# Kernel tuning notes

Measured on AMD Instinct MI355X. Metric: run time of the kernel, lower is better.

Reference implementation:

```python
import jax, jax.numpy as jnp
import numpy as np

E = 512
H = 8
HD = E // H  # head dim = 64


def setup_inputs() -> dict:
    key = jax.random.key(0)
    ks = jax.random.split(key, 7)
    B, P, R = 32, 4096, 64
    visual_tokens = jax.random.normal(ks[0], (B, P, E), dtype=jnp.float32)
    region_tokens = jax.random.normal(ks[1], (B, R, E), dtype=jnp.float32)
    distance_mask = jax.random.uniform(ks[2], (B, P, R), dtype=jnp.float32)
    s = 1.0 / np.sqrt(E)
    in_proj_weight = jax.random.uniform(ks[3], (3 * E, E), jnp.float32, -s, s)
    in_proj_bias = jnp.zeros((3 * E,), jnp.float32)
    out_proj_weight = jax.random.uniform(ks[4], (E, E), jnp.float32, -s, s)
    out_proj_bias = jnp.zeros((E,), jnp.float32)
    return {
        "visual_tokens": visual_tokens,
        "region_tokens": region_tokens,
        "distance_mask": distance_mask,
        "in_proj_weight": in_proj_weight,
        "in_proj_bias": in_proj_bias,
        "out_proj_weight": out_proj_weight,
        "out_proj_bias": out_proj_bias,
    }


def reference(visual_tokens, region_tokens, distance_mask,
              in_proj_weight, in_proj_bias, out_proj_weight, out_proj_bias):
    B, P, _ = visual_tokens.shape
    R = region_tokens.shape[1]
    # additive logit bias derived from distance mask (broadcast over heads,
    # instead of repeating B*H copies like the torch code)
    bias = (1.0 - distance_mask.astype(jnp.float32)) * -1e9  # [B,P,R]
    Wq, Wk, Wv = in_proj_weight[:E], in_proj_weight[E:2 * E], in_proj_weight[2 * E:]
    bq, bk, bv = in_proj_bias[:E], in_proj_bias[E:2 * E], in_proj_bias[2 * E:]
    v32 = visual_tokens.astype(jnp.float32)
    r32 = region_tokens.astype(jnp.float32)
    q = (v32 @ Wq.T + bq).reshape(B, P, H, HD)
    k = (r32 @ Wk.T + bk).reshape(B, R, H, HD)
    v = (r32 @ Wv.T + bv).reshape(B, R, H, HD)
    scale = 1.0 / jnp.sqrt(jnp.float32(HD))
    scores = jnp.einsum('bphd,brhd->bhpr', q, k) * scale + bias[:, None]  # [B,H,P,R]
    attn = jax.nn.softmax(scores, axis=-1)
    ctx = jnp.einsum('bhpr,brhd->bphd', attn, v).reshape(B, P, E)
    attended = ctx @ out_proj_weight.T + out_proj_bias
    return attended.astype(visual_tokens.dtype) + visual_tokens
```

## Files before the change

### kernel.cpp

```cpp
#include <hip/hip_runtime.h>
#include <hip/hip_bf16.h>

typedef unsigned short u16;
typedef unsigned int u32;

using bf16x8 = __attribute__((ext_vector_type(8))) short;
using f32x4  = __attribute__((ext_vector_type(4))) float;

#define MFMA16(a, b, c) __builtin_amdgcn_mfma_f32_16x16x32_bf16((a), (b), (c), 0, 0, 0)

__device__ __forceinline__ u16 f2bf(float f) {
    u32 u = __builtin_bit_cast(u32, f);
    u = (u + 0x7fffu + ((u >> 16) & 1u)) >> 16;
    return (u16)u;
}

__global__ __launch_bounds__(256, 2) void frgca_prep(
    const float* __restrict__ region,
    const float* __restrict__ in_w,
    const float* __restrict__ in_b,
    const float* __restrict__ out_w,
    u16* __restrict__ wq, u16* __restrict__ wo,
    u16* __restrict__ kt, u16* __restrict__ vt)
{
    __shared__ u16 As2[64 * 520];
    const int tid = threadIdx.x;
    const int bid = blockIdx.x;

    if (bid < 32) {
        const float4* w4q = (const float4*)in_w;
        const float4* w4o = (const float4*)out_w;
        int t = bid * 256 + tid;
#pragma unroll
        for (int i = 0; i < 16; ++i) {
            int idx = t + i * 8192;
            float4 v;
            u16* dst;
            if (idx < 65536) { v = w4q[idx]; dst = wq + idx * 4; }
            else             { v = w4o[idx - 65536]; dst = wo + (idx - 65536) * 4; }
            ushort4 o;
            o.x = f2bf(v.x); o.y = f2bf(v.y); o.z = f2bf(v.z); o.w = f2bf(v.w);
            *(ushort4*)dst = o;
        }
        return;
    }

    const int t2 = bid - 32;
    const int b  = t2 >> 2;
    const int nc = t2 & 3;

    {
        const float4* r4 = (const float4*)(region + (size_t)b * 64 * 512);
#pragma unroll
        for (int i = 0; i < 32; ++i) {
            int f4  = tid + i * 256;
            int row = f4 >> 7;
            int c4  = f4 & 127;
            float4 v = r4[f4];
            ushort4 o;
            o.x = f2bf(v.x); o.y = f2bf(v.y); o.z = f2bf(v.z); o.w = f2bf(v.w);
            *(ushort4*)&As2[row * 520 + c4 * 4] = o;
        }
    }
    __syncthreads();

    const int lane = tid & 63, w = tid >> 6;
    const int lo16 = lane & 15, g = lane >> 4;
    const int e0 = nc * 256 + w * 64;

    f32x4 acc[4][4];
#pragma unroll
    for (int mt = 0; mt < 4; ++mt)
#pragma unroll
        for (int nt = 0; nt < 4; ++nt)
            acc[mt][nt] = f32x4{0.f, 0.f, 0.f, 0.f};

    const float* w2 = in_w + 512 * 512;

#pragma unroll 2
    for (int ks = 0; ks < 16; ++ks) {
        const int kc = ks * 32 + 8 * g;
        bf16x8 a[4], bb[4];
#pragma unroll
        for (int mt = 0; mt < 4; ++mt)
            a[mt] = *(const bf16x8*)&As2[(mt * 16 + lo16) * 520 + kc];
#pragma unroll
        for (int nt = 0; nt < 4; ++nt) {
            const int e = e0 + nt * 16 + lo16;
            const float* src = w2 + (size_t)e * 512 + kc;
            float4 v0 = *(const float4*)src;
            float4 v1 = *(const float4*)(src + 4);
            bf16x8 bv;
            bv[0] = (short)f2bf(v0.x); bv[1] = (short)f2bf(v0.y);
            bv[2] = (short)f2bf(v0.z); bv[3] = (short)f2bf(v0.w);
            bv[4] = (short)f2bf(v1.x); bv[5] = (short)f2bf(v1.y);
            bv[6] = (short)f2bf(v1.z); bv[7] = (short)f2bf(v1.w);
            bb[nt] = bv;
        }
#pragma unroll
        for (int mt = 0; mt < 4; ++mt)
#pragma unroll
            for (int nt = 0; nt < 4; ++nt)
                acc[mt][nt] = MFMA16(a[mt], bb[nt], acc[mt][nt]);
    }

#pragma unroll
    for (int nt = 0; nt < 4; ++nt) {
        const int e = e0 + nt * 16 + lo16;
        const float bias = in_b[512 + e];
#pragma unroll
        for (int mt = 0; mt < 4; ++mt)
#pragma unroll
            for (int i = 0; i < 4; ++i) {
                const int r = mt * 16 + 4 * g + i;
                const u16 o = f2bf(acc[mt][nt][i] + bias);
                if (e < 512) {
                    const int h = e >> 6, d = e & 63;
                    kt[(((size_t)(b * 8 + h)) * 64 + r) * 64 + d] = o;
                } else {
                    const int e2 = e - 512;
                    const int h = e2 >> 6, d = e2 & 63;
                    vt[(((size_t)(b * 8 + h)) * 64 + d) * 64 + r] = o;
                }
            }
    }
}

__global__ __launch_bounds__(512, 4) void frgca_main(
    const float* __restrict__ visual,
    const float* __restrict__ mask,
    const float* __restrict__ in_b,
    const float* __restrict__ out_b,
    const u16* __restrict__ wq, const u16* __restrict__ wo,
    const u16* __restrict__ kt, const u16* __restrict__ vt,
    float* __restrict__ out)
{
    __shared__ char regA[65536];
    __shared__ float Ms[4096];

    const int tid = threadIdx.x;
    const int w = tid >> 6, lane = tid & 63;
    const int lo16 = lane & 15, g = lane >> 4;
    const int xr = (lo16 & 7) << 4;
    const int pt = blockIdx.x, b = blockIdx.y;
    const int P0 = pt * 64;
    const size_t vbase = ((size_t)(b * 4096 + P0)) * 512;

    {
        const float4* v4 = (const float4*)(visual + vbase);
#pragma unroll
        for (int i = 0; i < 16; ++i) {
            int f4  = tid + i * 512;
            int row = f4 >> 7, c4 = f4 & 127;
            float4 v = v4[f4];
            ushort4 o;
            o.x = f2bf(v.x); o.y = f2bf(v.y); o.z = f2bf(v.z); o.w = f2bf(v.w);
            *(ushort4*)(regA + row * 1024 + ((c4 * 8) ^ ((row & 7) << 4))) = o;
        }
        const float4* m4 = (const float4*)(mask + ((size_t)(b * 4096 + P0)) * 64);
#pragma unroll
        for (int i = 0; i < 2; ++i) {
            int f4 = tid + i * 512;
            int p = f4 >> 4, r0 = (f4 & 15) * 4;
            float4 v = m4[f4];
            int pb = p * 64, px = p & 31;
            Ms[pb + ((r0 + 0) ^ px)] = (1.0f - v.x) * -1e9f;
            Ms[pb + ((r0 + 1) ^ px)] = (1.0f - v.y) * -1e9f;
            Ms[pb + ((r0 + 2) ^ px)] = (1.0f - v.z) * -1e9f;
            Ms[pb + ((r0 + 3) ^ px)] = (1.0f - v.w) * -1e9f;
        }
    }
    __syncthreads();

    const int e0 = w * 64;

    f32x4 acc[4][4];
#pragma unroll
    for (int mt = 0; mt < 4; ++mt)
#pragma unroll
        for (int nt = 0; nt < 4; ++nt)
            acc[mt][nt] = f32x4{0.f, 0.f, 0.f, 0.f};

    const u16* wqR0 = wq + ((size_t)(e0 + 0 * 16 + lo16)) * 512;
    const u16* wqR1 = wq + ((size_t)(e0 + 1 * 16 + lo16)) * 512;
    const u16* wqR2 = wq + ((size_t)(e0 + 2 * 16 + lo16)) * 512;
    const u16* wqR3 = wq + ((size_t)(e0 + 3 * 16 + lo16)) * 512;
    bf16x8 nb0 = *(const bf16x8*)&wqR0[8 * g];
    bf16x8 nb1 = *(const bf16x8*)&wqR1[8 * g];
    bf16x8 nb2 = *(const bf16x8*)&wqR2[8 * g];
    bf16x8 nb3 = *(const bf16x8*)&wqR3[8 * g];

#pragma unroll
    for (int ks = 0; ks < 16; ++ks) {
        const int kc = ks * 32 + 8 * g;
        bf16x8 cb0 = nb0, cb1 = nb1, cb2 = nb2, cb3 = nb3;
        if (ks < 15) {
            const int kn = kc + 32;
            nb0 = *(const bf16x8*)&wqR0[kn];
            nb1 = *(const bf16x8*)&wqR1[kn];
            nb2 = *(const bf16x8*)&wqR2[kn];
            nb3 = *(const bf16x8*)&wqR3[kn];
        }
        bf16x8 a[4];
#pragma unroll
        for (int mt = 0; mt < 4; ++mt)
            a[mt] = *(const bf16x8*)(regA + (mt * 16 + lo16) * 1024 + ((kc * 2) ^ xr));
        acc[0][0] = MFMA16(a[0], cb0, acc[0][0]);
        acc[1][0] = MFMA16(a[1], cb0, acc[1][0]);
        acc[2][0] = MFMA16(a[2], cb0, acc[2][0]);
        acc[3][0] = MFMA16(a[3], cb0, acc[3][0]);
        acc[0][1] = MFMA16(a[0], cb1, acc[0][1]);
        acc[1][1] = MFMA16(a[1], cb1, acc[1][1]);
        acc[2][1] = MFMA16(a[2], cb1, acc[2][1]);
        acc[3][1] = MFMA16(a[3], cb1, acc[3][1]);
        acc[0][2] = MFMA16(a[0], cb2, acc[0][2]);
        acc[1][2] = MFMA16(a[1], cb2, acc[1][2]);
        acc[2][2] = MFMA16(a[2], cb2, acc[2][2]);
        acc[3][2] = MFMA16(a[3], cb2, acc[3][2]);
        acc[0][3] = MFMA16(a[0], cb3, acc[0][3]);
        acc[1][3] = MFMA16(a[1], cb3, acc[1][3]);
        acc[2][3] = MFMA16(a[2], cb3, acc[2][3]);
        acc[3][3] = MFMA16(a[3], cb3, acc[3][3]);
    }

    const u16* KtH = kt + ((size_t)(b * 8 + w)) * 4096;
    bf16x8 ak[4][2];
#pragma unroll
    for (int ks2 = 0; ks2 < 2; ++ks2)
#pragma unroll
        for (int mt = 0; mt < 4; ++mt)
            ak[mt][ks2] = *(const bf16x8*)&KtH[(mt * 16 + lo16) * 64 + ks2 * 32 + 8 * g];

#pragma unroll
    for (int nt = 0; nt < 4; ++nt) {
        const float bq = in_b[e0 + nt * 16 + lo16];
#pragma unroll
        for (int mt = 0; mt < 4; ++mt)
#pragma unroll
            for (int i = 0; i < 4; ++i)
                acc[mt][nt][i] += bq;
    }
    __syncthreads();

    char* Qw = regA + w * 8192;
#pragma unroll
    for (int mt = 0; mt < 4; ++mt)
#pragma unroll
        for (int nt = 0; nt < 4; ++nt)
#pragma unroll
            for (int i = 0; i < 4; ++i) {
                const int p = mt * 16 + 4 * g + i;
                const int d = nt * 16 + lo16;
                *(u16*)(Qw + p * 128 + ((d * 2) ^ ((p & 7) << 4))) = f2bf(acc[mt][nt][i]);
            }

    f32x4 s[4][4];
#pragma unroll
    for (int mt = 0; mt < 4; ++mt)
#pragma unroll
        for (int nt = 0; nt < 4; ++nt)
            s[mt][nt] = f32x4{0.f, 0.f, 0.f, 0.f};

#pragma unroll
    for (int ks2 = 0; ks2 < 2; ++ks2) {
        const int kcb = (ks2 * 32 + 8 * g) * 2;
        bf16x8 bq_[4];
#pragma unroll
        for (int nt = 0; nt < 4; ++nt)
            bq_[nt] = *(const bf16x8*)(Qw + (nt * 16 + lo16) * 128 + (kcb ^ xr));
#pragma unroll
        for (int mt = 0; mt < 4; ++mt)
#pragma unroll
            for (int nt = 0; nt < 4; ++nt)
                s[mt][nt] = MFMA16(ak[mt][ks2], bq_[nt], s[mt][nt]);
    }

    const u16* VtH = vt + ((size_t)(b * 8 + w)) * 4096;
    bf16x8 av[4][2];
#pragma unroll
    for (int ks2 = 0; ks2 < 2; ++ks2)
#pragma unroll
        for (int mt = 0; mt < 4; ++mt)
            av[mt][ks2] = *(const bf16x8*)&VtH[(mt * 16 + lo16) * 64 + ks2 * 32 + 8 * g];

#pragma unroll
    for (int nt = 0; nt < 4; ++nt) {
        const int p = nt * 16 + lo16;
        const int pb = p * 64, px = p & 31;
        float mx = -3.4e38f;
#pragma unroll
        for (int mt = 0; mt < 4; ++mt)
#pragma unroll
            for (int i = 0; i < 4; ++i) {
                float v = s[mt][nt][i] * 0.125f + Ms[pb + ((mt * 16 + 4 * g + i) ^ px)];
                s[mt][nt][i] = v;
                mx = fmaxf(mx, v);
            }
        mx = fmaxf(mx, __shfl_xor(mx, 16));
        mx = fmaxf(mx, __shfl_xor(mx, 32));
        float sum = 0.f;
#pragma unroll
        for (int mt = 0; mt < 4; ++mt)
#pragma unroll
            for (int i = 0; i < 4; ++i) {
                float ev = __expf(s[mt][nt][i] - mx);
                s[mt][nt][i] = ev;
                sum += ev;
            }
        sum += __shfl_xor(sum, 16);
        sum += __shfl_xor(sum, 32);
        const float inv = 1.0f / sum;
#pragma unroll
        for (int mt = 0; mt < 4; ++mt)
#pragma unroll
            for (int i = 0; i < 4; ++i) {
                const int r = mt * 16 + 4 * g + i;
                *(u16*)(Qw + p * 128 + ((r * 2) ^ ((p & 7) << 4))) = f2bf(s[mt][nt][i] * inv);
            }
    }

    f32x4 c_[4][4];
#pragma unroll
    for (int mt = 0; mt < 4; ++mt)
#pragma unroll
        for (int nt = 0; nt < 4; ++nt)
            c_[mt][nt] = f32x4{0.f, 0.f, 0.f, 0.f};

#pragma unroll
    for (int ks2 = 0; ks2 < 2; ++ks2) {
        const int kcb = (ks2 * 32 + 8 * g) * 2;
        bf16x8 bs_[4];
#pragma unroll
        for (int nt = 0; nt < 4; ++nt)
            bs_[nt] = *(const bf16x8*)(Qw + (nt * 16 + lo16) * 128 + (kcb ^ xr));
#pragma unroll
        for (int mt = 0; mt < 4; ++mt)
#pragma unroll
            for (int nt = 0; nt < 4; ++nt)
                c_[mt][nt] = MFMA16(av[mt][ks2], bs_[nt], c_[mt][nt]);
    }
    __syncthreads();

#pragma unroll
    for (int mt = 0; mt < 4; ++mt)
#pragma unroll
        for (int nt = 0; nt < 4; ++nt)
#pragma unroll
            for (int i = 0; i < 4; ++i) {
                const int p = nt * 16 + lo16;
                const int c = e0 + mt * 16 + 4 * g + i;
                *(u16*)(regA + p * 1024 + ((c * 2) ^ ((p & 7) << 4))) = f2bf(c_[mt][nt][i]);
            }
    __syncthreads();

    f32x4 o_[4][4];
#pragma unroll
    for (int mt = 0; mt < 4; ++mt)
#pragma unroll
        for (int nt = 0; nt < 4; ++nt)
            o_[mt][nt] = f32x4{0.f, 0.f, 0.f, 0.f};

    const u16* woR0 = wo + ((size_t)(e0 + 0 * 16 + lo16)) * 512;
    const u16* woR1 = wo + ((size_t)(e0 + 1 * 16 + lo16)) * 512;
    const u16* woR2 = wo + ((size_t)(e0 + 2 * 16 + lo16)) * 512;
    const u16* woR3 = wo + ((size_t)(e0 + 3 * 16 + lo16)) * 512;
    bf16x8 ob0 = *(const bf16x8*)&woR0[8 * g];
    bf16x8 ob1 = *(const bf16x8*)&woR1[8 * g];
    bf16x8 ob2 = *(const bf16x8*)&woR2[8 * g];
    bf16x8 ob3 = *(const bf16x8*)&woR3[8 * g];

#pragma unroll
    for (int ks = 0; ks < 16; ++ks) {
        const int kc = ks * 32 + 8 * g;
        bf16x8 cb0 = ob0, cb1 = ob1, cb2 = ob2, cb3 = ob3;
        if (ks < 15) {
            const int kn = kc + 32;
            ob0 = *(const bf16x8*)&woR0[kn];
            ob1 = *(const bf16x8*)&woR1[kn];
            ob2 = *(const bf16x8*)&woR2[kn];
            ob3 = *(const bf16x8*)&woR3[kn];
        }
        bf16x8 a[4];
#pragma unroll
        for (int mt = 0; mt < 4; ++mt)
            a[mt] = *(const bf16x8*)(regA + (mt * 16 + lo16) * 1024 + ((kc * 2) ^ xr));
        o_[0][0] = MFMA16(a[0], cb0, o_[0][0]);
        o_[1][0] = MFMA16(a[1], cb0, o_[1][0]);
        o_[2][0] = MFMA16(a[2], cb0, o_[2][0]);
        o_[3][0] = MFMA16(a[3], cb0, o_[3][0]);
        o_[0][1] = MFMA16(a[0], cb1, o_[0][1]);
        o_[1][1] = MFMA16(a[1], cb1, o_[1][1]);
        o_[2][1] = MFMA16(a[2], cb1, o_[2][1]);
        o_[3][1] = MFMA16(a[3], cb1, o_[3][1]);
        o_[0][2] = MFMA16(a[0], cb2, o_[0][2]);
        o_[1][2] = MFMA16(a[1], cb2, o_[1][2]);
        o_[2][2] = MFMA16(a[2], cb2, o_[2][2]);
        o_[3][2] = MFMA16(a[3], cb2, o_[3][2]);
        o_[0][3] = MFMA16(a[0], cb3, o_[0][3]);
        o_[1][3] = MFMA16(a[1], cb3, o_[1][3]);
        o_[2][3] = MFMA16(a[2], cb3, o_[2][3]);
        o_[3][3] = MFMA16(a[3], cb3, o_[3][3]);
    }

#pragma unroll
    for (int nt = 0; nt < 4; ++nt) {
        const int e = e0 + nt * 16 + lo16;
        const float bo = out_b[e];
#pragma unroll
        for (int mt = 0; mt < 4; ++mt)
#pragma unroll
            for (int i = 0; i < 4; ++i) {
                const int p = mt * 16 + 4 * g + i;
                const size_t gid = vbase + (size_t)p * 512 + e;
                out[gid] = o_[mt][nt][i] + bo + visual[gid];
            }
    }
}

extern "C" void kernel_launch(void* const* d_in, const int* in_sizes, int n_in,
                              void* d_out, int out_size, void* d_ws, size_t ws_size,
                              hipStream_t stream) {
    const float* visual = (const float*)d_in[0];
    const float* region = (const float*)d_in[1];
    const float* mask   = (const float*)d_in[2];
    const float* in_w   = (const float*)d_in[3];
    const float* in_b   = (const float*)d_in[4];
    const float* out_w  = (const float*)d_in[5];
    const float* out_b  = (const float*)d_in[6];
    float* out = (float*)d_out;

    char* ws = (char*)d_ws;
    u16* wq = (u16*)(ws + 0);
    u16* wo = (u16*)(ws + 524288);
    u16* kt = (u16*)(ws + 1048576);
    u16* vt = (u16*)(ws + 3145728);

    frgca_prep<<<dim3(160), dim3(256), 0, stream>>>(region, in_w, in_b, out_w, wq, wo, kt, vt);
    frgca_main<<<dim3(64, 32), dim3(512), 0, stream>>>(visual, mask, in_b, out_b, wq, wo, kt, vt, out);
}
```

Before: 483.2 us.

## Split fused attention kernel into separate attention and output-projection kernels

Splits the monolithic main kernel into two launches. The first computes the Q projection, masked softmax attention and context, and writes the bf16 context per head to a workspace buffer. The second reloads that context and runs the output projection plus residual. The aim is probably to ease register or LDS pressure per kernel, at the cost of a 128MB round-trip through global memory and an extra launch. The old fused path remains as a fallback when the workspace is too small.

Result: slower. 632.2 us (+30.8%).

```diff
diff --git a/kernel.cpp b/kernel.cpp
--- a/kernel.cpp
+++ b/kernel.cpp
@@ -126,6 +126,308 @@
     }
 }
 
+__global__ __launch_bounds__(512, 4) void frgca_qattn(
+    const float* __restrict__ visual,
+    const float* __restrict__ mask,
+    const float* __restrict__ in_b,
+    const u16* __restrict__ wq,
+    const u16* __restrict__ kt, const u16* __restrict__ vt,
+    u16* __restrict__ cb)
+{
+    __shared__ char regA[65536];
+    __shared__ float Ms[4096];
+
+    const int tid = threadIdx.x;
+    const int w = tid >> 6, lane = tid & 63;
+    const int lo16 = lane & 15, g = lane >> 4;
+    const int xr = (lo16 & 7) << 4;
+    const int pt = blockIdx.x, b = blockIdx.y;
+    const int P0 = pt * 64;
+    const size_t vbase = ((size_t)(b * 4096 + P0)) * 512;
+
+    {
+        const float4* v4 = (const float4*)(visual + vbase);
+#pragma unroll
+        for (int i = 0; i < 16; ++i) {
+            int f4  = tid + i * 512;
+            int row = f4 >> 7, c4 = f4 & 127;
+            float4 v = v4[f4];
+            ushort4 o;
+            o.x = f2bf(v.x); o.y = f2bf(v.y); o.z = f2bf(v.z); o.w = f2bf(v.w);
+            *(ushort4*)(regA + row * 1024 + ((c4 * 8) ^ ((row & 7) << 4))) = o;
+        }
+        const float4* m4 = (const float4*)(mask + ((size_t)(b * 4096 + P0)) * 64);
+#pragma unroll
+        for (int i = 0; i < 2; ++i) {
+            int f4 = tid + i * 512;
+            int p = f4 >> 4, r0 = (f4 & 15) * 4;
+            float4 v = m4[f4];
+            int pb = p * 64, px = p & 31;
+            Ms[pb + ((r0 + 0) ^ px)] = (1.0f - v.x) * -1e9f;
+            Ms[pb + ((r0 + 1) ^ px)] = (1.0f - v.y) * -1e9f;
+            Ms[pb + ((r0 + 2) ^ px)] = (1.0f - v.z) * -1e9f;
+            Ms[pb + ((r0 + 3) ^ px)] = (1.0f - v.w) * -1e9f;
+        }
+    }
+    __syncthreads();
+
+    const int e0 = w * 64;
+
+    f32x4 acc[4][4];
+#pragma unroll
+    for (int mt = 0; mt < 4; ++mt)
+#pragma unroll
+        for (int nt = 0; nt < 4; ++nt)
+            acc[mt][nt] = f32x4{0.f, 0.f, 0.f, 0.f};
+
+    const u16* wqR0 = wq + ((size_t)(e0 + 0 * 16 + lo16)) * 512;
+    const u16* wqR1 = wq + ((size_t)(e0 + 1 * 16 + lo16)) * 512;
+    const u16* wqR2 = wq + ((size_t)(e0 + 2 * 16 + lo16)) * 512;
+    const u16* wqR3 = wq + ((size_t)(e0 + 3 * 16 + lo16)) * 512;
+    bf16x8 nb0 = *(const bf16x8*)&wqR0[8 * g];
+    bf16x8 nb1 = *(const bf16x8*)&wqR1[8 * g];
+    bf16x8 nb2 = *(const bf16x8*)&wqR2[8 * g];
+    bf16x8 nb3 = *(const bf16x8*)&wqR3[8 * g];
+
+#pragma unroll
+    for (int ks = 0; ks < 16; ++ks) {
+        const int kc = ks * 32 + 8 * g;
+        bf16x8 cb0 = nb0, cb1 = nb1, cb2 = nb2, cb3 = nb3;
+        if (ks < 15) {
+            const int kn = kc + 32;
+            nb0 = *(const bf16x8*)&wqR0[kn];
+            nb1 = *(const bf16x8*)&wqR1[kn];
+            nb2 = *(const bf16x8*)&wqR2[kn];
+            nb3 = *(const bf16x8*)&wqR3[kn];
+        }
+        bf16x8 a[4];
+#pragma unroll
+        for (int mt = 0; mt < 4; ++mt)
+            a[mt] = *(const bf16x8*)(regA + (mt * 16 + lo16) * 1024 + ((kc * 2) ^ xr));
+#pragma unroll
+        for (int mt = 0; mt < 4; ++mt) {
+            acc[mt][0] = MFMA16(a[mt], cb0, acc[mt][0]);
+            acc[mt][1] = MFMA16(a[mt], cb1, acc[mt][1]);
+            acc[mt][2] = MFMA16(a[mt], cb2, acc[mt][2]);
+            acc[mt][3] = MFMA16(a[mt], cb3, acc[mt][3]);
+        }
+    }
+
+    const u16* KtH = kt + ((size_t)(b * 8 + w)) * 4096;
+    bf16x8 ak[4][2];
+#pragma unroll
+    for (int ks2 = 0; ks2 < 2; ++ks2)
+#pragma unroll
+        for (int mt = 0; mt < 4; ++mt)
+            ak[mt][ks2] = *(const bf16x8*)&KtH[(mt * 16 + lo16) * 64 + ks2 * 32 + 8 * g];
+
+#pragma unroll
+    for (int nt = 0; nt < 4; ++nt) {
+        const float bq = in_b[e0 + nt * 16 + lo16];
+#pragma unroll
+        for (int mt = 0; mt < 4; ++mt)
+#pragma unroll
+            for (int i = 0; i < 4; ++i)
+                acc[mt][nt][i] += bq;
+    }
+    __syncthreads();
+
+    char* Qw = regA + w * 8192;
+#pragma unroll
+    for (int mt = 0; mt < 4; ++mt)
+#pragma unroll
+        for (int nt = 0; nt < 4; ++nt)
+#pragma unroll
+            for (int i = 0; i < 4; ++i) {
+                const int p = mt * 16 + 4 * g + i;
+                const int d = nt * 16 + lo16;
+                *(u16*)(Qw + p * 128 + ((d * 2) ^ ((p & 7) << 4))) = f2bf(acc[mt][nt][i]);
+            }
+
+    f32x4 s[4][4];
+#pragma unroll
+    for (int mt = 0; mt < 4; ++mt)
+#pragma unroll
+        for (int nt = 0; nt < 4; ++nt)
+            s[mt][nt] = f32x4{0.f, 0.f, 0.f, 0.f};
+
+#pragma unroll
+    for (int ks2 = 0; ks2 < 2; ++ks2) {
+        const int kcb = (ks2 * 32 + 8 * g) * 2;
+        bf16x8 bq_[4];
+#pragma unroll
+        for (int nt = 0; nt < 4; ++nt)
+            bq_[nt] = *(const bf16x8*)(Qw + (nt * 16 + lo16) * 128 + (kcb ^ xr));
+#pragma unroll
+        for (int mt = 0; mt < 4; ++mt)
+#pragma unroll
+            for (int nt = 0; nt < 4; ++nt)
+                s[mt][nt] = MFMA16(ak[mt][ks2], bq_[nt], s[mt][nt]);
+    }
+
+    const u16* VtH = vt + ((size_t)(b * 8 + w)) * 4096;
+    bf16x8 av[4][2];
+#pragma unroll
+    for (int ks2 = 0; ks2 < 2; ++ks2)
+#pragma unroll
+        for (int mt = 0; mt < 4; ++mt)
+            av[mt][ks2] = *(const bf16x8*)&VtH[(mt * 16 + lo16) * 64 + ks2 * 32 + 8 * g];
+
+#pragma unroll
+    for (int nt = 0; nt < 4; ++nt) {
+        const int p = nt * 16 + lo16;
+        const int pb = p * 64, px = p & 31;
+        float mx = -3.4e38f;
+#pragma unroll
+        for (int mt = 0; mt < 4; ++mt)
+#pragma unroll
+            for (int i = 0; i < 4; ++i) {
+                float v = s[mt][nt][i] * 0.125f + Ms[pb + ((mt * 16 + 4 * g + i) ^ px)];
+                s[mt][nt][i] = v;
+                mx = fmaxf(mx, v);
+            }
+        mx = fmaxf(mx, __shfl_xor(mx, 16));
+        mx = fmaxf(mx, __shfl_xor(mx, 32));
+        float sum = 0.f;
+#pragma unroll
+        for (int mt = 0; mt < 4; ++mt)
+#pragma unroll
+            for (int i = 0; i < 4; ++i) {
+                float ev = __expf(s[mt][nt][i] - mx);
+                s[mt][nt][i] = ev;
+                sum += ev;
+            }
+        sum += __shfl_xor(sum, 16);
+        sum += __shfl_xor(sum, 32);
+        const float inv = 1.0f / sum;
+#pragma unroll
+        for (int mt = 0; mt < 4; ++mt)
+#pragma unroll
+            for (int i = 0; i < 4; ++i) {
+                const int r = mt * 16 + 4 * g + i;
+                *(u16*)(Qw + p * 128 + ((r * 2) ^ ((p & 7) << 4))) = f2bf(s[mt][nt][i] * inv);
+            }
+    }
+
+    f32x4 c_[4][4];
+#pragma unroll
+    for (int mt = 0; mt < 4; ++mt)
+#pragma unroll
+        for (int nt = 0; nt < 4; ++nt)
+            c_[mt][nt] = f32x4{0.f, 0.f, 0.f, 0.f};
+
+#pragma unroll
+    for (int ks2 = 0; ks2 < 2; ++ks2) {
+        const int kcb = (ks2 * 32 + 8 * g) * 2;
+        bf16x8 bs_[4];
+#pragma unroll
+        for (int nt = 0; nt < 4; ++nt)
+            bs_[nt] = *(const bf16x8*)(Qw + (nt * 16 + lo16) * 128 + (kcb ^ xr));
+#pragma unroll
+        for (int mt = 0; mt < 4; ++mt)
+#pragma unroll
+            for (int nt = 0; nt < 4; ++nt)
+                c_[mt][nt] = MFMA16(av[mt][ks2], bs_[nt], c_[mt][nt]);
+    }
+
+    {
+        const size_t cbase = ((size_t)(b * 8 + w) * 4096 + P0) * 64;
+#pragma unroll
+        for (int mt = 0; mt < 4; ++mt)
+#pragma unroll
+            for (int nt = 0; nt < 4; ++nt)
+#pragma unroll
+                for (int i = 0; i < 4; ++i) {
+                    const int d = mt * 16 + 4 * g + i;
+                    const int p = nt * 16 + lo16;
+                    cb[cbase + (size_t)p * 64 + d] = f2bf(c_[mt][nt][i]);
+                }
+    }
+}
+
+__global__ __launch_bounds__(512, 4) void frgca_oproj3(
+    const u16* __restrict__ cb, const u16* __restrict__ wo,
+    const float* __restrict__ out_b, const float* __restrict__ visual,
+    float* __restrict__ out)
+{
+    __shared__ char regA[65536];
+
+    const int tid = threadIdx.x;
+    const int w = tid >> 6, lane = tid & 63;
+    const int lo16 = lane & 15, g = lane >> 4;
+    const int xr = (lo16 & 7) << 4;
+    const int P0 = blockIdx.x * 64, b = blockIdx.y;
+    const size_t vbase = ((size_t)(b * 4096 + P0)) * 512;
+
+    {
+        const int p = tid >> 3;
+        const int h = tid & 7;
+        const u16* src = cb + ((size_t)(b * 8 + h) * 4096 + P0 + p) * 64;
+#pragma unroll
+        for (int d = 0; d < 64; ++d) {
+            const int c = h * 64 + d;
+            *(u16*)(regA + p * 1024 + ((c * 2) ^ ((p & 7) << 4))) = src[d];
+        }
+    }
+    __syncthreads();
+
+    const int e0 = w * 64;
+
+    f32x4 o_[4][4];
+#pragma unroll
+    for (int mt = 0; mt < 4; ++mt)
+#pragma unroll
+        for (int nt = 0; nt < 4; ++nt)
+            o_[mt][nt] = f32x4{0.f, 0.f, 0.f, 0.f};
+
+    const u16* woR0 = wo + ((size_t)(e0 + 0 * 16 + lo16)) * 512;
+    const u16* woR1 = wo + ((size_t)(e0 + 1 * 16 + lo16)) * 512;
+    const u16* woR2 = wo + ((size_t)(e0 + 2 * 16 + lo16)) * 512;
+    const u16* woR3 = wo + ((size_t)(e0 + 3 * 16 + lo16)) * 512;
+    bf16x8 ob0 = *(const bf16x8*)&woR0[8 * g];
+    bf16x8 ob1 = *(const bf16x8*)&woR1[8 * g];
+    bf16x8 ob2 = *(const bf16x8*)&woR2[8 * g];
+    bf16x8 ob3 = *(const bf16x8*)&woR3[8 * g];
+
+#pragma unroll
+    for (int ks = 0; ks < 16; ++ks) {
+        const int kc = ks * 32 + 8 * g;
+        bf16x8 cb0 = ob0, cb1 = ob1, cb2 = ob2, cb3 = ob3;
+        if (ks < 15) {
+            const int kn = kc + 32;
+            ob0 = *(const bf16x8*)&woR0[kn];
+            ob1 = *(const bf16x8*)&woR1[kn];
+            ob2 = *(const bf16x8*)&woR2[kn];
+            ob3 = *(const bf16x8*)&woR3[kn];
+        }
+        bf16x8 a[4];
+#pragma unroll
+        for (int mt = 0; mt < 4; ++mt)
+            a[mt] = *(const bf16x8*)(regA + (mt * 16 + lo16) * 1024 + ((kc * 2) ^ xr));
+#pragma unroll
+        for (int mt = 0; mt < 4; ++mt) {
+            o_[mt][0] = MFMA16(a[mt], cb0, o_[mt][0]);
+            o_[mt][1] = MFMA16(a[mt], cb1, o_[mt][1]);
+            o_[mt][2] = MFMA16(a[mt], cb2, o_[mt][2]);
+            o_[mt][3] = MFMA16(a[mt], cb3, o_[mt][3]);
+        }
+    }
+
+#pragma unroll
+    for (int nt = 0; nt < 4; ++nt) {
+        const int e = e0 + nt * 16 + lo16;
+        const float bo = out_b[e];
+#pragma unroll
+        for (int mt = 0; mt < 4; ++mt)
+#pragma unroll
+            for (int i = 0; i < 4; ++i) {
+                const int p = mt * 16 + 4 * g + i;
+                const size_t gid = vbase + (size_t)p * 512 + e;
+                out[gid] = o_[mt][nt][i] + bo + visual[gid];
+            }
+    }
+}
+
 __global__ __launch_bounds__(512, 4) void frgca_main(
     const float* __restrict__ visual,
     const float* __restrict__ mask,
@@ -205,22 +507,13 @@
 #pragma unroll
         for (int mt = 0; mt < 4; ++mt)
             a[mt] = *(const bf16x8*)(regA + (mt * 16 + lo16) * 1024 + ((kc * 2) ^ xr));
-        acc[0][0] = MFMA16(a[0], cb0, acc[0][0]);
-        acc[1][0] = MFMA16(a[1], cb0, acc[1][0]);
-        acc[2][0] = MFMA16(a[2], cb0, acc[2][0]);
-        acc[3][0] = MFMA16(a[3], cb0, acc[3][0]);
-        acc[0][1] = MFMA16(a[0], cb1, acc[0][1]);
-        acc[1][1] = MFMA16(a[1], cb1, acc[1][1]);
-        acc[2][1] = MFMA16(a[2], cb1, acc[2][1]);
-        acc[3][1] = MFMA16(a[3], cb1, acc[3][1]);
-        acc[0][2] = MFMA16(a[0], cb2, acc[0][2]);
-        acc[1][2] = MFMA16(a[1], cb2, acc[1][2]);
-        acc[2][2] = MFMA16(a[2], cb2, acc[2][2]);
-        acc[3][2] = MFMA16(a[3], cb2, acc[3][2]);
-        acc[0][3] = MFMA16(a[0], cb3, acc[0][3]);
-        acc[1][3] = MFMA16(a[1], cb3, acc[1][3]);
-        acc[2][3] = MFMA16(a[2], cb3, acc[2][3]);
-        acc[3][3] = MFMA16(a[3], cb3, acc[3][3]);
+#pragma unroll
+        for (int mt = 0; mt < 4; ++mt) {
+            acc[mt][0] = MFMA16(a[mt], cb0, acc[mt][0]);
+            acc[mt][1] = MFMA16(a[mt], cb1, acc[mt][1]);
+            acc[mt][2] = MFMA16(a[mt], cb2, acc[mt][2]);
+            acc[mt][3] = MFMA16(a[mt], cb3, acc[mt][3]);
+        }
     }
 
     const u16* KtH = kt + ((size_t)(b * 8 + w)) * 4096;
@@ -384,22 +677,13 @@
 #pragma unroll
         for (int mt = 0; mt < 4; ++mt)
             a[mt] = *(const bf16x8*)(regA + (mt * 16 + lo16) * 1024 + ((kc * 2) ^ xr));
-        o_[0][0] = MFMA16(a[0], cb0, o_[0][0]);
-        o_[1][0] = MFMA16(a[1], cb0, o_[1][0]);
-        o_[2][0] = MFMA16(a[2], cb0, o_[2][0]);
-        o_[3][0] = MFMA16(a[3], cb0, o_[3][0]);
-        o_[0][1] = MFMA16(a[0], cb1, o_[0][1]);
-        o_[1][1] = MFMA16(a[1], cb1, o_[1][1]);
-        o_[2][1] = MFMA16(a[2], cb1, o_[2][1]);
-        o_[3][1] = MFMA16(a[3], cb1, o_[3][1]);
-        o_[0][2] = MFMA16(a[0], cb2, o_[0][2]);
-        o_[1][2] = MFMA16(a[1], cb2, o_[1][2]);
-        o_[2][2] = MFMA16(a[2], cb2, o_[2][2]);
-        o_[3][2] = MFMA16(a[3], cb2, o_[3][2]);
-        o_[0][3] = MFMA16(a[0], cb3, o_[0][3]);
-        o_[1][3] = MFMA16(a[1], cb3, o_[1][3]);
-        o_[2][3] = MFMA16(a[2], cb3, o_[2][3]);
-        o_[3][3] = MFMA16(a[3], cb3, o_[3][3]);
+#pragma unroll
+        for (int mt = 0; mt < 4; ++mt) {
+            o_[mt][0] = MFMA16(a[mt], cb0, o_[mt][0]);
+            o_[mt][1] = MFMA16(a[mt], cb1, o_[mt][1]);
+            o_[mt][2] = MFMA16(a[mt], cb2, o_[mt][2]);
+            o_[mt][3] = MFMA16(a[mt], cb3, o_[mt][3]);
+        }
     }
 
 #pragma unroll
@@ -423,8 +707,8 @@
     const float* visual = (const float*)d_in[0];
     const float* region = (const float*)d_in[1];
     const float* mask   = (const float*)d_in[2];
+    const float* in_b   = (const float*)d_in[4];
     const float* in_w   = (const float*)d_in[3];
-    const float* in_b   = (const float*)d_in[4];
     const float* out_w  = (const float*)d_in[5];
     const float* out_b  = (const float*)d_in[6];
     float* out = (float*)d_out;
@@ -434,7 +718,15 @@
     u16* wo = (u16*)(ws + 524288);
     u16* kt = (u16*)(ws + 1048576);
     u16* vt = (u16*)(ws + 3145728);
+    u16* cbp = (u16*)(ws + 5242880);
+    const size_t REQ = 5242880ull + 134217728ull;
 
     frgca_prep<<<dim3(160), dim3(256), 0, stream>>>(region, in_w, in_b, out_w, wq, wo, kt, vt);
-    frgca_main<<<dim3(64, 32), dim3(512), 0, stream>>>(visual, mask, in_b, out_b, wq, wo, kt, vt, out);
+
+    if (ws_size >= REQ) {
+        frgca_qattn<<<dim3(64, 32), dim3(512), 0, stream>>>(visual, mask, in_b, wq, kt, vt, cbp);
+        frgca_oproj3<<<dim3(64, 32), dim3(512), 0, stream>>>(cbp, wo, out_b, visual, out);
+    } else {
+        frgca_main<<<dim3(64, 32), dim3(512), 0, stream>>>(visual, mask, in_b, out_b, wq, wo, kt, vt, out);
+    }
 }
```
